# Kernel optimization log

Measured on AMD Instinct MI355X. Metric: run time of the kernel, lower is better.

Reference implementation:

```python
import jax, jax.numpy as jnp
import numpy as np

B, OUT, IN = 1024, 512, 1024

def setup_inputs() -> dict:
    key = jax.random.key(0)
    k1, k2, k3, k4 = jax.random.split(key, 4)
    x = jax.random.uniform(k1, (B, IN), dtype=jnp.float32)            # inputs in [0,1]
    w = jax.random.uniform(k2, (OUT, IN), dtype=jnp.float32)          # centers in [min_input, max_input]=[0,1]
    u = jax.random.uniform(k3, (OUT, IN), dtype=jnp.float32, minval=0.2, maxval=0.7)  # slopes per init
    andor01 = jax.random.randint(k4, (1, OUT), 0, 2).astype(jnp.float32)  # frozen 0/1 mix ('*' mode)
    return {"x": x, "w": w, "u": u, "andor01": andor01}

def reference(x, w, u, andor01):
    # xuw = u * (x[b,None,i] - w[o,i]) ; z[b,o] = sum_i xuw^2 ; y = exp(-z)
    diff = u[None, :, :] * (x[:, None, :] - w[None, :, :])   # [B, OUT, IN]
    z = jnp.sum(diff * diff, axis=-1)                        # [B, OUT]
    y = jnp.exp(-z)                                          # forward of LargeAttractorExp
    # andor == '*': y + andor01 * (1 - 2y)
    return y + andor01 * (1.0 - 2.0 * y)
```

## Files before the change

### kernel.cpp

```cpp
#include <hip/hip_runtime.h>

#define B_SZ   1024
#define OUT_SZ 512
#define IN_SZ  1024
#define KK     2048

#define MB 64
#define NB 64
#define KSPLIT 8
#define KSL (KK / KSPLIT)
#define CH  64
#define NCH (KSL / CH)
#define NKC (KK / CH)
#define CHUNK_ENT 512

typedef __bf16 bf16x8 __attribute__((ext_vector_type(8)));
typedef float  f32x4  __attribute__((ext_vector_type(4)));

#define PART_BYTES ((size_t)KSPLIT * B_SZ * OUT_SZ * 4)
#define AIMG_OFF   PART_BYTES
#define AIMG_BYTES ((size_t)(B_SZ / MB) * NKC * CHUNK_ENT * 16)
#define BIMG_OFF   (AIMG_OFF + AIMG_BYTES)
#define BIMG_BYTES ((size_t)(OUT_SZ / NB) * NKC * CHUNK_ENT * 16)
#define RB_OFF     (BIMG_OFF + BIMG_BYTES)

__global__ __launch_bounds__(256) void rbf_prep(
    const float* __restrict__ x, const float* __restrict__ w,
    const float* __restrict__ u, __bf16* __restrict__ Aimg,
    __bf16* __restrict__ Bimg, float* __restrict__ rbias)
{
    const int bid = blockIdx.x, t = threadIdx.x;
    if (bid < 1024) {
        const int e    = (bid << 8) + t;
        const int slot = e & 63;
        const int frag = (e >> 6) & 3;
        const int s    = (e >> 8) & 1;
        const int kc   = (e >> 9) & 31;
        const int mT   = e >> 14;
        const int row  = mT * 64 + frag * 16 + (slot & 15);
        const int k0   = kc * 64 + s * 32 + (slot >> 4) * 8;
        const float* src = &x[(size_t)row * IN_SZ + (k0 & (IN_SZ - 1))];
        float4 v0 = *(const float4*)src;
        float4 v1 = *(const float4*)(src + 4);
        float vv[8] = {v0.x, v0.y, v0.z, v0.w, v1.x, v1.y, v1.z, v1.w};
        bf16x8 o8;
        if (k0 < IN_SZ) {
            #pragma unroll
            for (int j = 0; j < 8; ++j) o8[j] = (__bf16)(vv[j] * vv[j]);
        } else {
            #pragma unroll
            for (int j = 0; j < 8; ++j) o8[j] = (__bf16)vv[j];
        }
        *(bf16x8*)&Aimg[(size_t)e * 8] = o8;
    } else if (bid < 1536) {
        const int e    = ((bid - 1024) << 8) + t;
        const int slot = e & 63;
        const int frag = (e >> 6) & 3;
        const int s    = (e >> 8) & 1;
        const int kc   = (e >> 9) & 31;
        const int nT   = e >> 14;
        const int row  = nT * 64 + frag * 16 + (slot & 15);
        const int k0   = kc * 64 + s * 32 + (slot >> 4) * 8;
        const size_t off = (size_t)row * IN_SZ + (k0 & (IN_SZ - 1));
        float4 u0 = *(const float4*)&u[off];
        float4 u1 = *(const float4*)&u[off + 4];
        float uu[8] = {u0.x, u0.y, u0.z, u0.w, u1.x, u1.y, u1.z, u1.w};
        bf16x8 o8;
        if (k0 < IN_SZ) {
            #pragma unroll
            for (int j = 0; j < 8; ++j) o8[j] = (__bf16)(uu[j] * uu[j]);
        } else {
            float4 w0 = *(const float4*)&w[off];
            float4 w1 = *(const float4*)&w[off + 4];
            float ww[8] = {w0.x, w0.y, w0.z, w0.w, w1.x, w1.y, w1.z, w1.w};
            #pragma unroll
            for (int j = 0; j < 8; ++j) o8[j] = (__bf16)(-2.f * uu[j] * uu[j] * ww[j]);
        }
        *(bf16x8*)&Bimg[(size_t)e * 8] = o8;
    } else {
        const int o = ((bid - 1536) << 5) + (t >> 3);
        const size_t base = (size_t)o * IN_SZ + (size_t)(t & 7) * 128;
        float s = 0.f;
        for (int k2 = 0; k2 < 128; k2 += 4) {
            float4 uu = *(const float4*)&u[base + k2];
            float4 ww = *(const float4*)&w[base + k2];
            float p0 = uu.x * ww.x, p1 = uu.y * ww.y;
            float p2 = uu.z * ww.z, p3 = uu.w * ww.w;
            s = fmaf(p0, p0, s); s = fmaf(p1, p1, s);
            s = fmaf(p2, p2, s); s = fmaf(p3, p3, s);
        }
        s += __shfl_xor(s, 1);
        s += __shfl_xor(s, 2);
        s += __shfl_xor(s, 4);
        if ((t & 7) == 0) rbias[o] = s;
    }
}

__device__ __forceinline__ void gld_lds16(const __bf16* g, __bf16* l) {
    __builtin_amdgcn_global_load_lds(
        (const __attribute__((address_space(1))) void*)g,
        (__attribute__((address_space(3))) void*)l, 16, 0, 0);
}

__global__ __launch_bounds__(256) void rbf_gemm(
    const __bf16* __restrict__ Aimg, const __bf16* __restrict__ Bimg,
    float* __restrict__ part)
{
    __shared__ __bf16 Asm[2][CHUNK_ENT * 8];
    __shared__ __bf16 Bsm[2][CHUNK_ENT * 8];

    const int t = threadIdx.x, lane = t & 63;
    const int wv = t >> 6, wm = wv >> 1, wn = wv & 1;
    const int mT = blockIdx.x, nT = blockIdx.y, kz = blockIdx.z;

    f32x4 acc[2][2] = {};

    const __bf16* gA = &Aimg[(size_t)(mT * NKC + kz * NCH) * CHUNK_ENT * 8];
    const __bf16* gB = &Bimg[(size_t)(nT * NKC + kz * NCH) * CHUNK_ENT * 8];

    auto stage = [&](int buf, int c) {
        const __bf16* ga = gA + (size_t)c * CHUNK_ENT * 8;
        const __bf16* gb = gB + (size_t)c * CHUNK_ENT * 8;
        gld_lds16(ga + (size_t)t * 8,         &Asm[buf][t * 8]);
        gld_lds16(ga + (size_t)(t + 256) * 8, &Asm[buf][(t + 256) * 8]);
        gld_lds16(gb + (size_t)t * 8,         &Bsm[buf][t * 8]);
        gld_lds16(gb + (size_t)(t + 256) * 8, &Bsm[buf][(t + 256) * 8]);
    };

    stage(0, 0);
    #pragma unroll
    for (int c = 0; c < NCH; ++c) {
        __syncthreads();
        if (c + 1 < NCH) stage((c + 1) & 1, c + 1);
        const __bf16* Ab = Asm[c & 1];
        const __bf16* Bb = Bsm[c & 1];
        #pragma unroll
        for (int s = 0; s < 2; ++s) {
            bf16x8 a0 = *(const bf16x8*)&Ab[((s * 4 + wm * 2    ) * 64 + lane) * 8];
            bf16x8 a1 = *(const bf16x8*)&Ab[((s * 4 + wm * 2 + 1) * 64 + lane) * 8];
            bf16x8 b0 = *(const bf16x8*)&Bb[((s * 4 + wn * 2    ) * 64 + lane) * 8];
            bf16x8 b1 = *(const bf16x8*)&Bb[((s * 4 + wn * 2 + 1) * 64 + lane) * 8];
            acc[0][0] = __builtin_amdgcn_mfma_f32_16x16x32_bf16(a0, b0, acc[0][0], 0, 0, 0);
            acc[0][1] = __builtin_amdgcn_mfma_f32_16x16x32_bf16(a0, b1, acc[0][1], 0, 0, 0);
            acc[1][0] = __builtin_amdgcn_mfma_f32_16x16x32_bf16(a1, b0, acc[1][0], 0, 0, 0);
            acc[1][1] = __builtin_amdgcn_mfma_f32_16x16x32_bf16(a1, b1, acc[1][1], 0, 0, 0);
        }
    }

    const int col = lane & 15, rq = lane >> 4;
    #pragma unroll
    for (int mi = 0; mi < 2; ++mi) {
        const int b = mT * MB + (wm * 2 + mi) * 16 + rq * 4;
        #pragma unroll
        for (int ni = 0; ni < 2; ++ni) {
            const int o = nT * NB + (wn * 2 + ni) * 16 + col;
            #pragma unroll
            for (int r = 0; r < 4; ++r)
                part[((size_t)kz * B_SZ + (b + r)) * OUT_SZ + o] = acc[mi][ni][r];
        }
    }
}

__global__ __launch_bounds__(256) void rbf_reduce(
    const float* __restrict__ part, const float* __restrict__ rbias,
    const float* __restrict__ andor, float* __restrict__ out)
{
    const int i4   = blockIdx.x * 256 + threadIdx.x;
    const int base = i4 * 4;
    f32x4 z = {};
    #pragma unroll
    for (int kz = 0; kz < KSPLIT; ++kz)
        z += *(const f32x4*)&part[(size_t)kz * (B_SZ * OUT_SZ) + base];
    const int o = base & (OUT_SZ - 1);
    f32x4 rb = *(const f32x4*)&rbias[o];
    f32x4 av = *(const f32x4*)&andor[o];
    f32x4 res;
    #pragma unroll
    for (int j = 0; j < 4; ++j) {
        float y = __expf(-(z[j] + rb[j]));
        res[j] = fmaf(y, 1.f - 2.f * av[j], av[j]);
    }
    *(f32x4*)&out[base] = res;
}

extern "C" void kernel_launch(void* const* d_in, const int* in_sizes, int n_in,
                              void* d_out, int out_size, void* d_ws, size_t ws_size,
                              hipStream_t stream) {
    const float* x = (const float*)d_in[0];
    const float* w = (const float*)d_in[1];
    const float* u = (const float*)d_in[2];
    const float* a = (const float*)d_in[3];
    float* out = (float*)d_out;

    float*  part  = (float*)d_ws;
    __bf16* Aimg  = (__bf16*)((char*)d_ws + AIMG_OFF);
    __bf16* Bimg  = (__bf16*)((char*)d_ws + BIMG_OFF);
    float*  rbias = (float*)((char*)d_ws + RB_OFF);

    rbf_prep  <<<dim3(1552),      dim3(256), 0, stream>>>(x, w, u, Aimg, Bimg, rbias);
    rbf_gemm  <<<dim3(16, 8, 8),  dim3(256), 0, stream>>>(Aimg, Bimg, part);
    rbf_reduce<<<dim3(512),       dim3(256), 0, stream>>>(part, rbias, a, out);
}
```

Before: 84.28 us.

## Fuse split-K reduction into GEMM via last-block atomic, deepen LDS pipeline

Removes the separate reduce kernel. The last split-K block for each output tile, chosen with an atomic counter, sums the other partials and applies exp and the and/or mix directly. KSPLIT drops from 8 to 4, and the LDS staging becomes a 4-deep ring with explicit vmcnt waits and raw barriers. This saves a kernel launch and most of the partial-buffer traffic, but halves the grid, which lowers parallelism. It also adds a counter reset in prep and serialized tail work in the last block of each tile.

```diff
diff --git a/kernel.cpp b/kernel.cpp
--- a/kernel.cpp
+++ b/kernel.cpp
@@ -7,12 +7,13 @@
 
 #define MB 64
 #define NB 64
-#define KSPLIT 8
+#define KSPLIT 4
 #define KSL (KK / KSPLIT)
 #define CH  64
 #define NCH (KSL / CH)
 #define NKC (KK / CH)
 #define CHUNK_ENT 512
+#define DEPTH 4
 
 typedef __bf16 bf16x8 __attribute__((ext_vector_type(8)));
 typedef float  f32x4  __attribute__((ext_vector_type(4)));
@@ -23,11 +24,13 @@
 #define BIMG_OFF   (AIMG_OFF + AIMG_BYTES)
 #define BIMG_BYTES ((size_t)(OUT_SZ / NB) * NKC * CHUNK_ENT * 16)
 #define RB_OFF     (BIMG_OFF + BIMG_BYTES)
+#define CNT_OFF    (RB_OFF + OUT_SZ * 4)
 
 __global__ __launch_bounds__(256) void rbf_prep(
     const float* __restrict__ x, const float* __restrict__ w,
     const float* __restrict__ u, __bf16* __restrict__ Aimg,
-    __bf16* __restrict__ Bimg, float* __restrict__ rbias)
+    __bf16* __restrict__ Bimg, float* __restrict__ rbias,
+    int* __restrict__ cnt)
 {
     const int bid = blockIdx.x, t = threadIdx.x;
     if (bid < 1024) {
@@ -77,7 +80,7 @@
             for (int j = 0; j < 8; ++j) o8[j] = (__bf16)(-2.f * uu[j] * uu[j] * ww[j]);
         }
         *(bf16x8*)&Bimg[(size_t)e * 8] = o8;
-    } else {
+    } else if (bid < 1552) {
         const int o = ((bid - 1536) << 5) + (t >> 3);
         const size_t base = (size_t)o * IN_SZ + (size_t)(t & 7) * 128;
         float s = 0.f;
@@ -93,6 +96,8 @@
         s += __shfl_xor(s, 2);
         s += __shfl_xor(s, 4);
         if ((t & 7) == 0) rbias[o] = s;
+    } else {
+        if (t < (B_SZ / MB) * (OUT_SZ / NB)) cnt[t] = 0;
     }
 }
 
@@ -104,10 +109,13 @@
 
 __global__ __launch_bounds__(256) void rbf_gemm(
     const __bf16* __restrict__ Aimg, const __bf16* __restrict__ Bimg,
-    float* __restrict__ part)
+    float* __restrict__ part, const float* __restrict__ rbias,
+    const float* __restrict__ andor, int* __restrict__ cnt,
+    float* __restrict__ out)
 {
-    __shared__ __bf16 Asm[2][CHUNK_ENT * 8];
-    __shared__ __bf16 Bsm[2][CHUNK_ENT * 8];
+    __shared__ __bf16 Asm[DEPTH][CHUNK_ENT * 8];
+    __shared__ __bf16 Bsm[DEPTH][CHUNK_ENT * 8];
+    __shared__ int lastFlag;
 
     const int t = threadIdx.x, lane = t & 63;
     const int wv = t >> 6, wm = wv >> 1, wn = wv & 1;
@@ -127,13 +135,9 @@
         gld_lds16(gb + (size_t)(t + 256) * 8, &Bsm[buf][(t + 256) * 8]);
     };
 
-    stage(0, 0);
-    #pragma unroll
-    for (int c = 0; c < NCH; ++c) {
-        __syncthreads();
-        if (c + 1 < NCH) stage((c + 1) & 1, c + 1);
-        const __bf16* Ab = Asm[c & 1];
-        const __bf16* Bb = Bsm[c & 1];
+    auto compute = [&](int buf) {
+        const __bf16* Ab = Asm[buf];
+        const __bf16* Bb = Bsm[buf];
         #pragma unroll
         for (int s = 0; s < 2; ++s) {
             bf16x8 a0 = *(const bf16x8*)&Ab[((s * 4 + wm * 2    ) * 64 + lane) * 8];
@@ -145,7 +149,26 @@
             acc[1][0] = __builtin_amdgcn_mfma_f32_16x16x32_bf16(a1, b0, acc[1][0], 0, 0, 0);
             acc[1][1] = __builtin_amdgcn_mfma_f32_16x16x32_bf16(a1, b1, acc[1][1], 0, 0, 0);
         }
-    }
+    };
+
+    stage(0, 0);
+    stage(1, 1);
+    stage(2, 2);
+
+#define WAITV(N) asm volatile("s_waitcnt vmcnt(" #N ")" ::: "memory")
+#define STEP(c, N) do {                                                   \
+        WAITV(N);                           \
+        __builtin_amdgcn_s_barrier();       \
+        __builtin_amdgcn_sched_barrier(0);                                \
+        if ((c) + DEPTH - 1 < NCH)                                        \
+            stage(((c) + DEPTH - 1) & (DEPTH - 1), (c) + DEPTH - 1);      \
+        compute((c) & (DEPTH - 1));                                       \
+    } while (0)
+
+    STEP(0, 8); STEP(1, 8); STEP(2, 8); STEP(3, 8);
+    STEP(4, 8); STEP(5, 8); STEP(6, 4); STEP(7, 0);
+#undef STEP
+#undef WAITV
 
     const int col = lane & 15, rq = lane >> 4;
     #pragma unroll
@@ -159,28 +182,37 @@
                 part[((size_t)kz * B_SZ + (b + r)) * OUT_SZ + o] = acc[mi][ni][r];
         }
     }
-}
-
-__global__ __launch_bounds__(256) void rbf_reduce(
-    const float* __restrict__ part, const float* __restrict__ rbias,
-    const float* __restrict__ andor, float* __restrict__ out)
-{
-    const int i4   = blockIdx.x * 256 + threadIdx.x;
-    const int base = i4 * 4;
-    f32x4 z = {};
-    #pragma unroll
-    for (int kz = 0; kz < KSPLIT; ++kz)
-        z += *(const f32x4*)&part[(size_t)kz * (B_SZ * OUT_SZ) + base];
-    const int o = base & (OUT_SZ - 1);
-    f32x4 rb = *(const f32x4*)&rbias[o];
-    f32x4 av = *(const f32x4*)&andor[o];
-    f32x4 res;
-    #pragma unroll
-    for (int j = 0; j < 4; ++j) {
-        float y = __expf(-(z[j] + rb[j]));
-        res[j] = fmaf(y, 1.f - 2.f * av[j], av[j]);
+    __threadfence();
+    __syncthreads();
+    if (t == 0)
+        lastFlag = (atomicAdd(&cnt[mT * (OUT_SZ / NB) + nT], 1) == KSPLIT - 1);
+    __syncthreads();
+
+    if (lastFlag) {
+        __threadfence();
+        #pragma unroll
+        for (int mi = 0; mi < 2; ++mi) {
+            const int b = mT * MB + (wm * 2 + mi) * 16 + rq * 4;
+            #pragma unroll
+            for (int ni = 0; ni < 2; ++ni) {
+                const int o = nT * NB + (wn * 2 + ni) * 16 + col;
+                const float rb = rbias[o];
+                const float a  = andor[o];
+                const float cf = 1.f - 2.f * a;
+                #pragma unroll
+                for (int r = 0; r < 4; ++r) {
+                    float z = acc[mi][ni][r] + rb;
+                    #pragma unroll
+                    for (int k2 = 0; k2 < KSPLIT; ++k2)
+                        if (k2 != kz)
+                            z += *(const volatile float*)
+                                 &part[((size_t)k2 * B_SZ + (b + r)) * OUT_SZ + o];
+                    float y = __expf(-z);
+                    out[(size_t)(b + r) * OUT_SZ + o] = fmaf(y, cf, a);
+                }
+            }
+        }
     }
-    *(f32x4*)&out[base] = res;
 }
 
 extern "C" void kernel_launch(void* const* d_in, const int* in_sizes, int n_in,
@@ -196,8 +228,9 @@
     __bf16* Aimg  = (__bf16*)((char*)d_ws + AIMG_OFF);
     __bf16* Bimg  = (__bf16*)((char*)d_ws + BIMG_OFF);
     float*  rbias = (float*)((char*)d_ws + RB_OFF);
-
-    rbf_prep  <<<dim3(1552),      dim3(256), 0, stream>>>(x, w, u, Aimg, Bimg, rbias);
-    rbf_gemm  <<<dim3(16, 8, 8),  dim3(256), 0, stream>>>(Aimg, Bimg, part);
-    rbf_reduce<<<dim3(512),       dim3(256), 0, stream>>>(part, rbias, a, out);
-}
+    int*    cnt   = (int*)((char*)d_ws + CNT_OFF);
+
+    rbf_prep<<<dim3(1553), dim3(256), 0, stream>>>(x, w, u, Aimg, Bimg, rbias, cnt);
+    rbf_gemm<<<dim3(B_SZ / MB, OUT_SZ / NB, KSPLIT), dim3(256), 0, stream>>>(
+        Aimg, Bimg, part, rbias, a, cnt, out);
+}
```

Result: slower. 153.9 us (+82.6%).

## Drop split-K and fuse the exp epilogue into a 32x32-tile GEMM

Applied to the files above, without the earlier changes.

Removes the 8-way split-K partial buffer and the separate reduce kernel. The GEMM now uses 32x32 output tiles over the full K range and applies the bias, exp and and/or mix directly in its epilogue. Staging moves from direct global-to-LDS async loads to register prefetch plus LDS stores with two barriers per chunk. The prep kernel is also restructured to read rows coalesced, 16 floats per thread. This eliminates about 16 MB of partial-sum traffic and one launch, at the cost of a longer serial K loop with a single MFMA accumulator per wave and more barriers.

```diff
diff --git a/kernel.cpp b/kernel.cpp
--- a/kernel.cpp
+++ b/kernel.cpp
@@ -3,25 +3,19 @@
 #define B_SZ   1024
 #define OUT_SZ 512
 #define IN_SZ  1024
-#define KK     2048
 
-#define MB 64
-#define NB 64
-#define KSPLIT 8
-#define KSL (KK / KSPLIT)
-#define CH  64
-#define NCH (KSL / CH)
-#define NKC (KK / CH)
+#define NKC 32
 #define CHUNK_ENT 512
+
+#define MBT 32
+#define NBT 32
 
 typedef __bf16 bf16x8 __attribute__((ext_vector_type(8)));
 typedef float  f32x4  __attribute__((ext_vector_type(4)));
 
-#define PART_BYTES ((size_t)KSPLIT * B_SZ * OUT_SZ * 4)
-#define AIMG_OFF   PART_BYTES
-#define AIMG_BYTES ((size_t)(B_SZ / MB) * NKC * CHUNK_ENT * 16)
-#define BIMG_OFF   (AIMG_OFF + AIMG_BYTES)
-#define BIMG_BYTES ((size_t)(OUT_SZ / NB) * NKC * CHUNK_ENT * 16)
+#define AIMG_BYTES ((size_t)16 * NKC * CHUNK_ENT * 16)
+#define BIMG_OFF   AIMG_BYTES
+#define BIMG_BYTES ((size_t)8  * NKC * CHUNK_ENT * 16)
 #define RB_OFF     (BIMG_OFF + BIMG_BYTES)
 
 __global__ __launch_bounds__(256) void rbf_prep(
@@ -30,55 +24,58 @@
     __bf16* __restrict__ Bimg, float* __restrict__ rbias)
 {
     const int bid = blockIdx.x, t = threadIdx.x;
-    if (bid < 1024) {
-        const int e    = (bid << 8) + t;
-        const int slot = e & 63;
-        const int frag = (e >> 6) & 3;
-        const int s    = (e >> 8) & 1;
-        const int kc   = (e >> 9) & 31;
-        const int mT   = e >> 14;
-        const int row  = mT * 64 + frag * 16 + (slot & 15);
-        const int k0   = kc * 64 + s * 32 + (slot >> 4) * 8;
-        const float* src = &x[(size_t)row * IN_SZ + (k0 & (IN_SZ - 1))];
-        float4 v0 = *(const float4*)src;
-        float4 v1 = *(const float4*)(src + 4);
-        float vv[8] = {v0.x, v0.y, v0.z, v0.w, v1.x, v1.y, v1.z, v1.w};
-        bf16x8 o8;
-        if (k0 < IN_SZ) {
+    if (bid < 768) {
+        const bool isA = bid < 512;
+        const int  rel = isA ? bid : bid - 512;
+        const int  tile = rel >> 5, kc = rel & 31;
+        const int  r = t >> 2, c4 = t & 3;
+        const int  row = tile * 64 + r;
+        const int  kb  = (kc & 15) * 64 + c4 * 16;
+        const bool firstHalf = (kc < 16);
+
+        float f[16];
+        __bf16 g[16];
+        if (isA) {
+            const float4* src = (const float4*)&x[(size_t)row * IN_SZ + kb];
             #pragma unroll
-            for (int j = 0; j < 8; ++j) o8[j] = (__bf16)(vv[j] * vv[j]);
+            for (int q = 0; q < 4; ++q) *(float4*)&f[q * 4] = src[q];
+            if (firstHalf) {
+                #pragma unroll
+                for (int j = 0; j < 16; ++j) g[j] = (__bf16)(f[j] * f[j]);
+            } else {
+                #pragma unroll
+                for (int j = 0; j < 16; ++j) g[j] = (__bf16)f[j];
+            }
         } else {
+            const float4* su = (const float4*)&u[(size_t)row * IN_SZ + kb];
             #pragma unroll
-            for (int j = 0; j < 8; ++j) o8[j] = (__bf16)vv[j];
+            for (int q = 0; q < 4; ++q) *(float4*)&f[q * 4] = su[q];
+            if (firstHalf) {
+                #pragma unroll
+                for (int j = 0; j < 16; ++j) g[j] = (__bf16)(f[j] * f[j]);
+            } else {
+                float fw[16];
+                const float4* sw = (const float4*)&w[(size_t)row * IN_SZ + kb];
+                #pragma unroll
+                for (int q = 0; q < 4; ++q) *(float4*)&fw[q * 4] = sw[q];
+                #pragma unroll
+                for (int j = 0; j < 16; ++j)
+                    g[j] = (__bf16)(-2.f * f[j] * f[j] * fw[j]);
+            }
         }
-        *(bf16x8*)&Aimg[(size_t)e * 8] = o8;
-    } else if (bid < 1536) {
-        const int e    = ((bid - 1024) << 8) + t;
-        const int slot = e & 63;
-        const int frag = (e >> 6) & 3;
-        const int s    = (e >> 8) & 1;
-        const int kc   = (e >> 9) & 31;
-        const int nT   = e >> 14;
-        const int row  = nT * 64 + frag * 16 + (slot & 15);
-        const int k0   = kc * 64 + s * 32 + (slot >> 4) * 8;
-        const size_t off = (size_t)row * IN_SZ + (k0 & (IN_SZ - 1));
-        float4 u0 = *(const float4*)&u[off];
-        float4 u1 = *(const float4*)&u[off + 4];
-        float uu[8] = {u0.x, u0.y, u0.z, u0.w, u1.x, u1.y, u1.z, u1.w};
-        bf16x8 o8;
-        if (k0 < IN_SZ) {
+        __bf16* dst = (isA ? Aimg : Bimg) + (size_t)rel * CHUNK_ENT * 8;
+        #pragma unroll
+        for (int h = 0; h < 2; ++h) {
+            const int idx2 = c4 * 2 + h;
+            const int s = idx2 >> 2, quad = idx2 & 3;
+            const int e = (s * 4 + (r >> 4)) * 64 + quad * 16 + (r & 15);
+            bf16x8 o8;
             #pragma unroll
-            for (int j = 0; j < 8; ++j) o8[j] = (__bf16)(uu[j] * uu[j]);
-        } else {
-            float4 w0 = *(const float4*)&w[off];
-            float4 w1 = *(const float4*)&w[off + 4];
-            float ww[8] = {w0.x, w0.y, w0.z, w0.w, w1.x, w1.y, w1.z, w1.w};
-            #pragma unroll
-            for (int j = 0; j < 8; ++j) o8[j] = (__bf16)(-2.f * uu[j] * uu[j] * ww[j]);
+            for (int j = 0; j < 8; ++j) o8[j] = g[h * 8 + j];
+            *(bf16x8*)&dst[(size_t)e * 8] = o8;
         }
-        *(bf16x8*)&Bimg[(size_t)e * 8] = o8;
     } else {
-        const int o = ((bid - 1536) << 5) + (t >> 3);
+        const int o = ((bid - 768) << 5) + (t >> 3);
         const size_t base = (size_t)o * IN_SZ + (size_t)(t & 7) * 128;
         float s = 0.f;
         for (int k2 = 0; k2 < 128; k2 += 4) {
@@ -96,91 +93,61 @@
     }
 }
 
-__device__ __forceinline__ void gld_lds16(const __bf16* g, __bf16* l) {
-    __builtin_amdgcn_global_load_lds(
-        (const __attribute__((address_space(1))) void*)g,
-        (__attribute__((address_space(3))) void*)l, 16, 0, 0);
-}
-
 __global__ __launch_bounds__(256) void rbf_gemm(
     const __bf16* __restrict__ Aimg, const __bf16* __restrict__ Bimg,
-    float* __restrict__ part)
+    const float* __restrict__ rbias, const float* __restrict__ andor,
+    float* __restrict__ out)
 {
-    __shared__ __bf16 Asm[2][CHUNK_ENT * 8];
-    __shared__ __bf16 Bsm[2][CHUNK_ENT * 8];
+    __shared__ __bf16 Asm[256 * 8];
+    __shared__ __bf16 Bsm[256 * 8];
 
     const int t = threadIdx.x, lane = t & 63;
     const int wv = t >> 6, wm = wv >> 1, wn = wv & 1;
-    const int mT = blockIdx.x, nT = blockIdx.y, kz = blockIdx.z;
+    const int mT = blockIdx.x;
+    const int nT = blockIdx.y;
+    const int fbA = (mT & 1) * 2;
+    const int fbB = (nT & 1) * 2;
 
-    f32x4 acc[2][2] = {};
+    const __bf16* gA = Aimg + (size_t)(mT >> 1) * NKC * CHUNK_ENT * 8;
+    const __bf16* gB = Bimg + (size_t)(nT >> 1) * NKC * CHUNK_ENT * 8;
 
-    const __bf16* gA = &Aimg[(size_t)(mT * NKC + kz * NCH) * CHUNK_ENT * 8];
-    const __bf16* gB = &Bimg[(size_t)(nT * NKC + kz * NCH) * CHUNK_ENT * 8];
+    const int sE = t >> 7, fiE = (t >> 6) & 1, slE = t & 63;
+    const int eA = (((sE * 4 + fbA + fiE) * 64 + slE)) * 8;
+    const int eB = (((sE * 4 + fbB + fiE) * 64 + slE)) * 8;
 
-    auto stage = [&](int buf, int c) {
-        const __bf16* ga = gA + (size_t)c * CHUNK_ENT * 8;
-        const __bf16* gb = gB + (size_t)c * CHUNK_ENT * 8;
-        gld_lds16(ga + (size_t)t * 8,         &Asm[buf][t * 8]);
-        gld_lds16(ga + (size_t)(t + 256) * 8, &Asm[buf][(t + 256) * 8]);
-        gld_lds16(gb + (size_t)t * 8,         &Bsm[buf][t * 8]);
-        gld_lds16(gb + (size_t)(t + 256) * 8, &Bsm[buf][(t + 256) * 8]);
+    f32x4 acc = {};
+    bf16x8 ra, rb;
+    auto load = [&](int c) {
+        ra = *(const bf16x8*)&gA[(size_t)c * CHUNK_ENT * 8 + eA];
+        rb = *(const bf16x8*)&gB[(size_t)c * CHUNK_ENT * 8 + eB];
     };
 
-    stage(0, 0);
-    #pragma unroll
-    for (int c = 0; c < NCH; ++c) {
+    load(0);
+    for (int c = 0; c < NKC; ++c) {
+        if (c) __syncthreads();
+        *(bf16x8*)&Asm[t * 8] = ra;
+        *(bf16x8*)&Bsm[t * 8] = rb;
         __syncthreads();
-        if (c + 1 < NCH) stage((c + 1) & 1, c + 1);
-        const __bf16* Ab = Asm[c & 1];
-        const __bf16* Bb = Bsm[c & 1];
+        if (c + 1 < NKC) load(c + 1);
         #pragma unroll
         for (int s = 0; s < 2; ++s) {
-            bf16x8 a0 = *(const bf16x8*)&Ab[((s * 4 + wm * 2    ) * 64 + lane) * 8];
-            bf16x8 a1 = *(const bf16x8*)&Ab[((s * 4 + wm * 2 + 1) * 64 + lane) * 8];
-            bf16x8 b0 = *(const bf16x8*)&Bb[((s * 4 + wn * 2    ) * 64 + lane) * 8];
-            bf16x8 b1 = *(const bf16x8*)&Bb[((s * 4 + wn * 2 + 1) * 64 + lane) * 8];
-            acc[0][0] = __builtin_amdgcn_mfma_f32_16x16x32_bf16(a0, b0, acc[0][0], 0, 0, 0);
-            acc[0][1] = __builtin_amdgcn_mfma_f32_16x16x32_bf16(a0, b1, acc[0][1], 0, 0, 0);
-            acc[1][0] = __builtin_amdgcn_mfma_f32_16x16x32_bf16(a1, b0, acc[1][0], 0, 0, 0);
-            acc[1][1] = __builtin_amdgcn_mfma_f32_16x16x32_bf16(a1, b1, acc[1][1], 0, 0, 0);
+            bf16x8 av = *(const bf16x8*)&Asm[((s * 2 + wm) * 64 + lane) * 8];
+            bf16x8 bv = *(const bf16x8*)&Bsm[((s * 2 + wn) * 64 + lane) * 8];
+            acc = __builtin_amdgcn_mfma_f32_16x16x32_bf16(av, bv, acc, 0, 0, 0);
         }
     }
 
     const int col = lane & 15, rq = lane >> 4;
+    const int b = mT * MBT + wm * 16 + rq * 4;
+    const int o = nT * NBT + wn * 16 + col;
+    const float rbv = rbias[o];
+    const float a   = andor[o];
+    const float cf  = 1.f - 2.f * a;
     #pragma unroll
-    for (int mi = 0; mi < 2; ++mi) {
-        const int b = mT * MB + (wm * 2 + mi) * 16 + rq * 4;
-        #pragma unroll
-        for (int ni = 0; ni < 2; ++ni) {
-            const int o = nT * NB + (wn * 2 + ni) * 16 + col;
-            #pragma unroll
-            for (int r = 0; r < 4; ++r)
-                part[((size_t)kz * B_SZ + (b + r)) * OUT_SZ + o] = acc[mi][ni][r];
-        }
+    for (int r = 0; r < 4; ++r) {
+        float y = __expf(-(acc[r] + rbv));
+        out[(size_t)(b + r) * OUT_SZ + o] = fmaf(y, cf, a);
     }
-}
-
-__global__ __launch_bounds__(256) void rbf_reduce(
-    const float* __restrict__ part, const float* __restrict__ rbias,
-    const float* __restrict__ andor, float* __restrict__ out)
-{
-    const int i4   = blockIdx.x * 256 + threadIdx.x;
-    const int base = i4 * 4;
-    f32x4 z = {};
-    #pragma unroll
-    for (int kz = 0; kz < KSPLIT; ++kz)
-        z += *(const f32x4*)&part[(size_t)kz * (B_SZ * OUT_SZ) + base];
-    const int o = base & (OUT_SZ - 1);
-    f32x4 rb = *(const f32x4*)&rbias[o];
-    f32x4 av = *(const f32x4*)&andor[o];
-    f32x4 res;
-    #pragma unroll
-    for (int j = 0; j < 4; ++j) {
-        float y = __expf(-(z[j] + rb[j]));
-        res[j] = fmaf(y, 1.f - 2.f * av[j], av[j]);
-    }
-    *(f32x4*)&out[base] = res;
 }
 
 extern "C" void kernel_launch(void* const* d_in, const int* in_sizes, int n_in,
@@ -192,12 +159,11 @@
     const float* a = (const float*)d_in[3];
     float* out = (float*)d_out;
 
-    float*  part  = (float*)d_ws;
-    __bf16* Aimg  = (__bf16*)((char*)d_ws + AIMG_OFF);
+    __bf16* Aimg  = (__bf16*)d_ws;
     __bf16* Bimg  = (__bf16*)((char*)d_ws + BIMG_OFF);
     float*  rbias = (float*)((char*)d_ws + RB_OFF);
 
-    rbf_prep  <<<dim3(1552),      dim3(256), 0, stream>>>(x, w, u, Aimg, Bimg, rbias);
-    rbf_gemm  <<<dim3(16, 8, 8),  dim3(256), 0, stream>>>(Aimg, Bimg, part);
-    rbf_reduce<<<dim3(512),       dim3(256), 0, stream>>>(part, rbias, a, out);
+    rbf_prep<<<dim3(784), dim3(256), 0, stream>>>(x, w, u, Aimg, Bimg, rbias);
+    rbf_gemm<<<dim3(B_SZ / MBT, OUT_SZ / NBT), dim3(256), 0, stream>>>(
+        Aimg, Bimg, rbias, a, out);
 }
```

Measured after the change: 86.56 us. 2.7% more time.
